# Kernel tuning notes

Hardware: AMD Instinct MI355X
Metric: run time of the kernel (lower is better)

## Reference

```python
import jax, jax.numpy as jnp
import numpy as np

B, N, K, D, H = 16384, 10, 5, 512, 2
HD = D // H  # 256
IMG = 512.0


def setup_inputs() -> dict:
    key = jax.random.key(0)
    ks = jax.random.split(key, 18)
    w = lambda k, shape: (jax.random.normal(k, shape) * 0.02).astype(jnp.float32)
    boxes = jax.random.uniform(ks[0], (B, N, 4), minval=0.0, maxval=IMG, dtype=jnp.float32)
    return {
        'boxes': boxes,
        'w_in': w(ks[1], (D, K * 4)), 'b_in': jnp.zeros((D,), jnp.float32),
        'wqkv': w(ks[2], (3 * D, D)), 'bqkv': jnp.zeros((3 * D,), jnp.float32),
        'wo': w(ks[3], (D, D)), 'bo': jnp.zeros((D,), jnp.float32),
        'ln1_w': jnp.ones((D,), jnp.float32), 'ln1_b': jnp.zeros((D,), jnp.float32),
        'w1': w(ks[4], (D, D)), 'b1': jnp.zeros((D,), jnp.float32),
        'w2': w(ks[5], (D, D)), 'b2': jnp.zeros((D,), jnp.float32),
        'ln2_w': jnp.ones((D,), jnp.float32), 'ln2_b': jnp.zeros((D,), jnp.float32),
        'lnf_w': jnp.ones((D,), jnp.float32), 'lnf_b': jnp.zeros((D,), jnp.float32),
    }


def _ln(x, w, b, eps=1e-5):
    mu = jnp.mean(x, -1, keepdims=True)
    var = jnp.mean((x - mu) ** 2, -1, keepdims=True)
    return (x - mu) * jax.lax.rsqrt(var + eps) * w + b


def _relationships(boxes):
    # boxes: [B, N, 4] -> rel: [B, N, K*4]
    cx = (boxes[..., 0] + boxes[..., 2]) * 0.5 / IMG
    cy = (boxes[..., 1] + boxes[..., 3]) * 0.5 / IMG
    bw = jnp.abs(boxes[..., 2] - boxes[..., 0]) / IMG
    bh = jnp.abs(boxes[..., 3] - boxes[..., 1]) / IMG
    feats = jnp.stack([cx, cy, bw, bh], -1)  # [B, N, 4]
    dx = cx[:, :, None] - cx[:, None, :]
    dy = cy[:, :, None] - cy[:, None, :]
    dists = dx * dx + dy * dy  # [B, N, N]
    dists = jnp.where(jnp.eye(N, dtype=bool), jnp.inf, dists)
    _, idx = jax.lax.top_k(-dists, K)  # K smallest, ascending -> [B, N, K]
    nbr = jnp.take_along_axis(jnp.broadcast_to(feats[:, None], (B, N, N, 4)), idx[:, :, :, None], axis=2)  # [B, N, K, 4]
    return (nbr - feats[:, :, None, :]).reshape(B, N, K * 4)


def reference(boxes, w_in, b_in, wqkv, bqkv, wo, bo, ln1_w, ln1_b, w1, b1, w2, b2, ln2_w, ln2_b, lnf_w, lnf_b):
    rel = _relationships(boxes)                      # [B, N, 20]
    x = rel @ w_in.T + b_in                          # [B, N, D]
    # --- self attention (post-norm TransformerEncoderLayer, eval mode: no dropout) ---
    qkv = x @ wqkv.T + bqkv
    q, k, v = jnp.split(qkv, 3, axis=-1)
    split_heads = lambda t: t.reshape(B, N, H, HD).transpose(0, 2, 1, 3)
    q, k, v = split_heads(q), split_heads(k), split_heads(v)
    scores = jnp.einsum('bhqd,bhkd->bhqk', q, k) / jnp.sqrt(jnp.float32(HD))
    att = jax.nn.softmax(scores, axis=-1)
    o = jnp.einsum('bhqk,bhkd->bhqd', att, v).transpose(0, 2, 1, 3).reshape(B, N, D)
    x = _ln(x + o @ wo.T + bo, ln1_w, ln1_b)
    # --- feed forward ---
    ff = jax.nn.gelu(x @ w1.T + b1, approximate=False) @ w2.T + b2
    x = _ln(x + ff, ln2_w, ln2_b)
    return _ln(x, lnf_w, lnf_b)
```

## Files before the change

### kernel.cpp

```cpp
#include <hip/hip_runtime.h>
#include <hip/hip_bf16.h>
#include <math.h>

#define B_   16384
#define NT   10
#define KNN  5
#define D_   512
#define MTOT (B_*NT)

typedef __bf16 bf;
typedef __bf16 bfrag8 __attribute__((ext_vector_type(8)));
typedef float  floatx4 __attribute__((ext_vector_type(4)));

__device__ __forceinline__ float tof(bf x) { return (float)x; }
__device__ __forceinline__ bf    tob(float x) { return (bf)x; }

#define GLD_LDS(g, l) __builtin_amdgcn_global_load_lds( \
    (const __attribute__((address_space(1))) void*)(g), \
    (__attribute__((address_space(3))) void*)(l), 16, 0, 0)

__global__ void prep_folds(const float* __restrict__ wqkv, const float* __restrict__ bqkv,
                           const float* __restrict__ wo,   const float* __restrict__ bo,
                           bf* __restrict__ At, bf* __restrict__ Ct,
                           float* __restrict__ wconst, float* __restrict__ uvec)
{
    int gid = blockIdx.x, tid = threadIdx.x;
    if (gid < 4096) {
        int idx = gid * 256 + tid;
        int mat = idx >> 18;
        int rem = idx & 262143;
        int row = rem >> 9, col = rem & 511;
        float acc = 0.f;
        if (mat < 2) {
            int h = mat;
            const float* wq = wqkv + (size_t)(h * 256) * 512;
            const float* wk = wqkv + (size_t)(512 + h * 256) * 512;
            for (int c = 0; c < 256; ++c)
                acc += wq[c * 512 + col] * wk[c * 512 + row];
            At[(size_t)h * 262144 + row * 512 + col] = tob(acc * 0.0625f);
        } else {
            int h = mat - 2;
            const float* wv = wqkv + (size_t)(1024 + h * 256) * 512;
            for (int e = 0; e < 256; ++e)
                acc += wv[e * 512 + col] * wo[row * 512 + h * 256 + e];
            Ct[(size_t)h * 262144 + row * 512 + col] = tob(acc);
        }
    } else {
        for (int d = tid; d < 512; d += 256) {
            float acc = bo[d];
            for (int e = 0; e < 512; ++e)
                acc += bqkv[1024 + e] * wo[d * 512 + e];
            wconst[d] = acc;
            for (int h = 0; h < 2; ++h) {
                float u = 0.f;
                for (int c = 0; c < 256; ++c)
                    u += wqkv[(size_t)(512 + h * 256 + c) * 512 + d] * bqkv[h * 256 + c];
                uvec[h * 512 + d] = u * 0.0625f;
            }
        }
    }
}

__global__ void cvt_w(const float* __restrict__ src, bf* __restrict__ dst)
{
    int i = blockIdx.x * 256 + threadIdx.x;
    float4 v = *(const float4*)(src + (size_t)i * 4);
    bf o[4] = { tob(v.x), tob(v.y), tob(v.z), tob(v.w) };
    *(unsigned long long*)(dst + (size_t)i * 4) = *(unsigned long long*)o;
}

__global__ void rel_kernel(const float* __restrict__ boxes, float* __restrict__ rel)
{
#pragma clang fp contract(off)
    int gid = blockIdx.x * blockDim.x + threadIdx.x;
    if (gid >= MTOT) return;
    int b = gid / NT, n = gid % NT;
    const float* bx = boxes + (size_t)b * NT * 4;
    float cx[NT], cy[NT], bw[NT], bh[NT];
#pragma unroll
    for (int j = 0; j < NT; ++j) {
        float x0 = bx[j * 4 + 0], y0 = bx[j * 4 + 1];
        float x1 = bx[j * 4 + 2], y1 = bx[j * 4 + 3];
        cx[j] = ((x0 + x1) * 0.5f) * (1.f / 512.f);
        cy[j] = ((y0 + y1) * 0.5f) * (1.f / 512.f);
        bw[j] = fabsf(x1 - x0) * (1.f / 512.f);
        bh[j] = fabsf(y1 - y0) * (1.f / 512.f);
    }
    float dist[NT];
#pragma unroll
    for (int j = 0; j < NT; ++j) {
        float dx = cx[n] - cx[j], dy = cy[n] - cy[j];
        float dxx = dx * dx, dyy = dy * dy;
        dist[j] = (j == n) ? __builtin_inff() : (dxx + dyy);
    }
    float ocx = cx[n], ocy = cy[n], obw = bw[n], obh = bh[n];
#pragma unroll
    for (int k = 0; k < KNN; ++k) {
        int best = 0; float bd = __builtin_inff();
#pragma unroll
        for (int j = 0; j < NT; ++j)
            if (dist[j] < bd) { bd = dist[j]; best = j; }
        float fx = 0, fy = 0, fw = 0, fh = 0;
#pragma unroll
        for (int j = 0; j < NT; ++j)
            if (j == best) { fx = cx[j]; fy = cy[j]; fw = bw[j]; fh = bh[j]; dist[j] = __builtin_inff(); }
        size_t o = (size_t)gid * 20 + k * 4;
        rel[o + 0] = fx - ocx;
        rel[o + 1] = fy - ocy;
        rel[o + 2] = fw - obw;
        rel[o + 3] = fh - obh;
    }
}

__global__ void gemm_in(const float* __restrict__ rel, const float* __restrict__ w_in,
                        const float* __restrict__ b_in, bf* __restrict__ x0)
{
    __shared__ __align__(16) float relS[128][20];
    int tid = threadIdx.x;
    size_t tok0 = (size_t)blockIdx.x * 128;
    for (int i = tid; i < 128 * 20; i += 256)
        relS[i / 20][i % 20] = rel[tok0 * 20 + i];
    float w0[20], w1r[20];
#pragma unroll
    for (int j = 0; j < 20; ++j) {
        w0[j]  = w_in[tid * 20 + j];
        w1r[j] = w_in[(tid + 256) * 20 + j];
    }
    float bias0 = b_in[tid], bias1 = b_in[tid + 256];
    __syncthreads();
    for (int tk = 0; tk < 128; ++tk) {
        const float4* rp = (const float4*)relS[tk];
        float a0 = bias0, a1 = bias1;
#pragma unroll
        for (int v4 = 0; v4 < 5; ++v4) {
            float4 rv = rp[v4];
            a0 += rv.x * w0[v4 * 4 + 0] + rv.y * w0[v4 * 4 + 1]
                + rv.z * w0[v4 * 4 + 2] + rv.w * w0[v4 * 4 + 3];
            a1 += rv.x * w1r[v4 * 4 + 0] + rv.y * w1r[v4 * 4 + 1]
                + rv.z * w1r[v4 * 4 + 2] + rv.w * w1r[v4 * 4 + 3];
        }
        x0[(tok0 + tk) * 512 + tid]       = tob(a0);
        x0[(tok0 + tk) * 512 + tid + 256] = tob(a1);
    }
}

template <int EPI>
__launch_bounds__(512, 4)
__global__ void gemm2(const bf* __restrict__ A, const bf* __restrict__ Bt,
                      bf* __restrict__ out, const float* __restrict__ biasf)
{
    __shared__ __align__(16) bf As[2][4096];
    __shared__ __align__(16) bf Bs[2][8192];
    int tid = threadIdx.x;
    int w = tid >> 6, l = tid & 63;
    int lq = l >> 4, lr = l & 15;
    size_t m0 = (size_t)blockIdx.y * 128;
    int n0 = blockIdx.x * 256;
    int wm = (w & 1) * 64, wn = (w >> 1) * 64;
    floatx4 acc[4][4] = {};

    const bf* Ag = A + (m0 + (size_t)(tid & 127)) * 512 + (tid >> 7) * 8;
    const bf* Bg = Bt + (size_t)(n0 + (tid & 255)) * 512 + (tid >> 8) * 8;

    auto stage = [&](int buf, int kt) {
        GLD_LDS(Ag + kt * 32,      &As[buf][w * 512]);
        GLD_LDS(Bg + kt * 32,      &Bs[buf][w * 512]);
        GLD_LDS(Bg + kt * 32 + 16, &Bs[buf][4096 + w * 512]);
    };

    stage(0, 0);
#pragma unroll 2
    for (int kt = 0; kt < 16; ++kt) {
        int cur = kt & 1;
        if (kt < 15) {
            stage(cur ^ 1, kt + 1);
            asm volatile("s_waitcnt vmcnt(3)" ::: "memory");
        } else {
            asm volatile("s_waitcnt vmcnt(0)" ::: "memory");
        }
        __builtin_amdgcn_sched_barrier(0);
        __builtin_amdgcn_s_barrier();
        __builtin_amdgcn_sched_barrier(0);

        const bf* as = &As[cur][(lq * 128 + wm + lr) * 8];
        const bf* bs = &Bs[cur][(lq * 256 + wn + lr) * 8];
        bfrag8 af[4], bfv[4];
#pragma unroll
        for (int i = 0; i < 4; ++i) af[i] = *(const bfrag8*)(as + i * 128);
#pragma unroll
        for (int j = 0; j < 4; ++j) bfv[j] = *(const bfrag8*)(bs + j * 128);
#pragma unroll
        for (int i = 0; i < 4; ++i)
#pragma unroll
            for (int j = 0; j < 4; ++j)
                acc[i][j] = __builtin_amdgcn_mfma_f32_16x16x32_bf16(af[i], bfv[j], acc[i][j], 0, 0, 0);

        if (kt < 15) {
            __builtin_amdgcn_sched_barrier(0);
            __builtin_amdgcn_s_barrier();
        }
    }

#pragma unroll
    for (int i = 0; i < 4; ++i)
#pragma unroll
        for (int j = 0; j < 4; ++j) {
            int col = n0 + wn + j * 16 + lr;
#pragma unroll
            for (int r = 0; r < 4; ++r) {
                size_t row = m0 + wm + i * 16 + lq * 4 + r;
                float v = acc[i][j][r];
                if (EPI == 1) { v += biasf[col]; v = 0.5f * v * (1.f + erff(v * 0.70710678118654752f)); }
                if (EPI == 2) v += biasf[col];
                if (EPI == 3) v += tof(out[row * 512 + col]);
                out[row * 512 + col] = tob(v);
            }
        }
}

__global__ void scoresz(bf* __restrict__ t, const bf* __restrict__ x0,
                        const float* __restrict__ uvec_h)
{
    __shared__ float as[4][256];
    int tid = threadIdx.x;
    int w = tid >> 6, l = tid & 63;
    int lq = l >> 4, lr = l & 15;
    size_t b = (size_t)blockIdx.x * 4 + w;
    bf* trow = t + (b * NT + lr) * 512;
    const bf* xrow = x0 + (b * NT + lr) * 512;
    floatx4 acc = {0.f, 0.f, 0.f, 0.f};
    float xu = 0.f;
#pragma unroll
    for (int kk = 0; kk < 16; ++kk) {
        bfrag8 a  = *(const bfrag8*)(trow + kk * 32 + lq * 8);
        bfrag8 bb = *(const bfrag8*)(xrow + kk * 32 + lq * 8);
        acc = __builtin_amdgcn_mfma_f32_16x16x32_bf16(a, bb, acc, 0, 0, 0);
#pragma unroll
        for (int jj = 0; jj < 8; ++jj)
            xu += (float)bb[jj] * uvec_h[kk * 32 + lq * 8 + jj];
    }
    xu += __shfl_xor(xu, 16);
    xu += __shfl_xor(xu, 32);
    bool jvalid = (lr < NT);
#pragma unroll
    for (int r = 0; r < 4; ++r) {
        float v = jvalid ? (acc[r] + xu) : -__builtin_inff();
        float m = v;
        m = fmaxf(m, __shfl_xor(m, 1)); m = fmaxf(m, __shfl_xor(m, 2));
        m = fmaxf(m, __shfl_xor(m, 4)); m = fmaxf(m, __shfl_xor(m, 8));
        float e = jvalid ? __expf(v - m) : 0.f;
        float s = e;
        s += __shfl_xor(s, 1); s += __shfl_xor(s, 2);
        s += __shfl_xor(s, 4); s += __shfl_xor(s, 8);
        float a = e / s;
        as[w][(lq * 4 + r) * 16 + lr] = a;
    }
    __syncthreads();
    bfrag8 xj[NT];
#pragma unroll
    for (int j = 0; j < NT; ++j)
        xj[j] = *(const bfrag8*)(x0 + (b * NT + j) * 512 + l * 8);
#pragma unroll
    for (int i = 0; i < NT; ++i) {
        float z[8] = {};
#pragma unroll
        for (int j = 0; j < NT; ++j) {
            float a = as[w][i * 16 + j];
#pragma unroll
            for (int q = 0; q < 8; ++q) z[q] += a * (float)xj[j][q];
        }
        bfrag8 zv;
#pragma unroll
        for (int q = 0; q < 8; ++q) zv[q] = tob(z[q]);
        *(bfrag8*)(t + (b * NT + i) * 512 + l * 8) = zv;
    }
}

__global__ void ln_kernel(const bf* __restrict__ xin, const bf* __restrict__ yin,
                          const float* __restrict__ w, const float* __restrict__ bias,
                          bf* __restrict__ xout)
{
    int tid = threadIdx.x;
    int wv = tid >> 6, l = tid & 63;
    size_t tok = (size_t)blockIdx.x * 4 + wv;
    bfrag8 xv = *(const bfrag8*)(xin + tok * 512 + l * 8);
    bfrag8 yv = *(const bfrag8*)(yin + tok * 512 + l * 8);
    float v[8]; float s = 0.f;
#pragma unroll
    for (int i = 0; i < 8; ++i) { v[i] = (float)xv[i] + (float)yv[i]; s += v[i]; }
#pragma unroll
    for (int m = 1; m < 64; m <<= 1) s += __shfl_xor(s, m);
    float mu = s * (1.f / 512.f);
    float vs = 0.f;
#pragma unroll
    for (int i = 0; i < 8; ++i) { float d = v[i] - mu; vs += d * d; }
#pragma unroll
    for (int m = 1; m < 64; m <<= 1) vs += __shfl_xor(vs, m);
    float r = rsqrtf(vs * (1.f / 512.f) + 1e-5f);
    bfrag8 ov;
#pragma unroll
    for (int i = 0; i < 8; ++i) {
        int d = l * 8 + i;
        ov[i] = tob((v[i] - mu) * r * w[d] + bias[d]);
    }
    *(bfrag8*)(xout + tok * 512 + l * 8) = ov;
}

__global__ void final_kernel(const bf* __restrict__ x1, const bf* __restrict__ ff2,
                             const float* __restrict__ w2, const float* __restrict__ b2,
                             const float* __restrict__ wf, const float* __restrict__ bfi,
                             float* __restrict__ out)
{
    int tid = threadIdx.x;
    int wv = tid >> 6, l = tid & 63;
    size_t tok = (size_t)blockIdx.x * 4 + wv;
    bfrag8 xv = *(const bfrag8*)(x1 + tok * 512 + l * 8);
    bfrag8 yv = *(const bfrag8*)(ff2 + tok * 512 + l * 8);
    float v[8]; float s = 0.f;
#pragma unroll
    for (int i = 0; i < 8; ++i) { v[i] = (float)xv[i] + (float)yv[i]; s += v[i]; }
#pragma unroll
    for (int m = 1; m < 64; m <<= 1) s += __shfl_xor(s, m);
    float mu = s * (1.f / 512.f);
    float vs = 0.f;
#pragma unroll
    for (int i = 0; i < 8; ++i) { float d = v[i] - mu; vs += d * d; }
#pragma unroll
    for (int m = 1; m < 64; m <<= 1) vs += __shfl_xor(vs, m);
    float r = rsqrtf(vs * (1.f / 512.f) + 1e-5f);
    float u[8]; float s2 = 0.f;
#pragma unroll
    for (int i = 0; i < 8; ++i) {
        int d = l * 8 + i;
        u[i] = (v[i] - mu) * r * w2[d] + b2[d];
        s2 += u[i];
    }
#pragma unroll
    for (int m = 1; m < 64; m <<= 1) s2 += __shfl_xor(s2, m);
    float mu2 = s2 * (1.f / 512.f);
    float vs2 = 0.f;
#pragma unroll
    for (int i = 0; i < 8; ++i) { float d = u[i] - mu2; vs2 += d * d; }
#pragma unroll
    for (int m = 1; m < 64; m <<= 1) vs2 += __shfl_xor(vs2, m);
    float r2 = rsqrtf(vs2 * (1.f / 512.f) + 1e-5f);
    float4 o0, o1;
    float* op = (float*)&o0;
#pragma unroll
    for (int i = 0; i < 4; ++i) op[i] = (u[i] - mu2) * r2 * wf[l * 8 + i] + bfi[l * 8 + i];
    op = (float*)&o1;
#pragma unroll
    for (int i = 0; i < 4; ++i) op[i] = (u[4 + i] - mu2) * r2 * wf[l * 8 + 4 + i] + bfi[l * 8 + 4 + i];
    *(float4*)(out + tok * 512 + l * 8) = o0;
    *(float4*)(out + tok * 512 + l * 8 + 4) = o1;
}

extern "C" void kernel_launch(void* const* d_in, const int* in_sizes, int n_in,
                              void* d_out, int out_size, void* d_ws, size_t ws_size,
                              hipStream_t stream)
{
    const float* boxes = (const float*)d_in[0];
    const float* w_in  = (const float*)d_in[1];
    const float* b_in  = (const float*)d_in[2];
    const float* wqkv  = (const float*)d_in[3];
    const float* bqkv  = (const float*)d_in[4];
    const float* wo    = (const float*)d_in[5];
    const float* bo    = (const float*)d_in[6];
    const float* ln1w  = (const float*)d_in[7];
    const float* ln1b  = (const float*)d_in[8];
    const float* w1    = (const float*)d_in[9];
    const float* b1    = (const float*)d_in[10];
    const float* w2    = (const float*)d_in[11];
    const float* b2    = (const float*)d_in[12];
    const float* ln2w  = (const float*)d_in[13];
    const float* ln2b  = (const float*)d_in[14];
    const float* lnfw  = (const float*)d_in[15];
    const float* lnfb  = (const float*)d_in[16];
    float* out = (float*)d_out;

    char* ws = (char*)d_ws;
    bf*    At     = (bf*)(ws + 0);
    bf*    Ct     = (bf*)(ws + 1048576);
    bf*    W1b    = (bf*)(ws + 2097152);
    bf*    W2b    = (bf*)(ws + 2621440);
    float* wconst = (float*)(ws + 3145728);
    float* uvec   = (float*)(ws + 3147776);
    bf*    x0     = (bf*)(ws + 16259072);
    bf*    t      = (bf*)(ws + 184047616);
    bf*    y      = (bf*)(ws + 351836160);
    float* rel    = (float*)(ws + 184047616);

    dim3 gblk(256);
    dim3 ggemm(2, MTOT / 128);

    prep_folds<<<4097, gblk, 0, stream>>>(wqkv, bqkv, wo, bo, At, Ct, wconst, uvec);
    cvt_w<<<256, gblk, 0, stream>>>(w1, W1b);
    cvt_w<<<256, gblk, 0, stream>>>(w2, W2b);
    rel_kernel<<<(MTOT + 255) / 256, gblk, 0, stream>>>(boxes, rel);
    gemm_in<<<MTOT / 128, gblk, 0, stream>>>(rel, w_in, b_in, x0);

    gemm2<0><<<ggemm, 512, 0, stream>>>(x0, At, t, nullptr);
    scoresz<<<B_ / 4, gblk, 0, stream>>>(t, x0, uvec);
    gemm2<2><<<ggemm, 512, 0, stream>>>(t, Ct, y, wconst);
    gemm2<0><<<ggemm, 512, 0, stream>>>(x0, At + 262144, t, nullptr);
    scoresz<<<B_ / 4, gblk, 0, stream>>>(t, x0, uvec + 512);
    gemm2<3><<<ggemm, 512, 0, stream>>>(t, Ct + 262144, y, nullptr);
    ln_kernel<<<MTOT / 4, gblk, 0, stream>>>(x0, y, ln1w, ln1b, x0);
    gemm2<1><<<ggemm, 512, 0, stream>>>(x0, W1b, t, b1);
    gemm2<2><<<ggemm, 512, 0, stream>>>(t, W2b, y, b2);
    final_kernel<<<MTOT / 4, gblk, 0, stream>>>(x0, y, ln2w, ln2b, lnfw, lnfb, out);
}
```

Before: 2.172 ms.

## Triple-buffer GEMM LDS staging and drop the trailing per-iteration barrier

Changes the bf16 MFMA GEMM from double to triple LDS buffering, issuing global-to-LDS loads two k-tiles ahead right after the single barrier and removing the second barrier in each iteration. LDS fragment reads become explicit ds_read_b128 with an lgkmcnt wait, and wave priority is raised around the MFMA block. This is meant to hide load latency and cut barrier stalls. The larger LDS footprint (72KB per block) may reduce how many blocks fit on each CU.

```diff
diff --git a/kernel.cpp b/kernel.cpp
--- a/kernel.cpp
+++ b/kernel.cpp
@@ -18,6 +18,13 @@
 #define GLD_LDS(g, l) __builtin_amdgcn_global_load_lds( \
     (const __attribute__((address_space(1))) void*)(g), \
     (__attribute__((address_space(3))) void*)(l), 16, 0, 0)
+
+__device__ __forceinline__ bfrag8 lds_read16(const bf* p) {
+    bfrag8 r;
+    unsigned a = (unsigned)(unsigned long long)(const __attribute__((address_space(3))) bf*)p;
+    asm volatile("ds_read_b128 %0, %1" : "=v"(r) : "v"(a));
+    return r;
+}
 
 __global__ void prep_folds(const float* __restrict__ wqkv, const float* __restrict__ bqkv,
                            const float* __restrict__ wo,   const float* __restrict__ bo,
@@ -146,11 +153,11 @@
 
 template <int EPI>
 __launch_bounds__(512, 4)
-__global__ void gemm2(const bf* __restrict__ A, const bf* __restrict__ Bt,
+__global__ void gemm3(const bf* __restrict__ A, const bf* __restrict__ Bt,
                       bf* __restrict__ out, const float* __restrict__ biasf)
 {
-    __shared__ __align__(16) bf As[2][4096];
-    __shared__ __align__(16) bf Bs[2][8192];
+    __shared__ __align__(16) bf As[3][4096];
+    __shared__ __align__(16) bf Bs[3][8192];
     int tid = threadIdx.x;
     int w = tid >> 6, l = tid & 63;
     int lq = l >> 4, lr = l & 15;
@@ -169,11 +176,10 @@
     };
 
     stage(0, 0);
-#pragma unroll 2
+    stage(1, 1);
+    int cur = 0;
     for (int kt = 0; kt < 16; ++kt) {
-        int cur = kt & 1;
         if (kt < 15) {
-            stage(cur ^ 1, kt + 1);
             asm volatile("s_waitcnt vmcnt(3)" ::: "memory");
         } else {
             asm volatile("s_waitcnt vmcnt(0)" ::: "memory");
@@ -182,23 +188,29 @@
         __builtin_amdgcn_s_barrier();
         __builtin_amdgcn_sched_barrier(0);
 
+        if (kt < 14) {
+            int nb = cur + 2; if (nb >= 3) nb -= 3;
+            stage(nb, kt + 2);
+        }
+
         const bf* as = &As[cur][(lq * 128 + wm + lr) * 8];
         const bf* bs = &Bs[cur][(lq * 256 + wn + lr) * 8];
         bfrag8 af[4], bfv[4];
 #pragma unroll
-        for (int i = 0; i < 4; ++i) af[i] = *(const bfrag8*)(as + i * 128);
-#pragma unroll
-        for (int j = 0; j < 4; ++j) bfv[j] = *(const bfrag8*)(bs + j * 128);
+        for (int i = 0; i < 4; ++i) af[i] = lds_read16(as + i * 128);
+#pragma unroll
+        for (int j = 0; j < 4; ++j) bfv[j] = lds_read16(bs + j * 128);
+        asm volatile("s_waitcnt lgkmcnt(0)" ::: "memory");
+        __builtin_amdgcn_sched_barrier(0);
+        __builtin_amdgcn_s_setprio(1);
 #pragma unroll
         for (int i = 0; i < 4; ++i)
 #pragma unroll
             for (int j = 0; j < 4; ++j)
                 acc[i][j] = __builtin_amdgcn_mfma_f32_16x16x32_bf16(af[i], bfv[j], acc[i][j], 0, 0, 0);
-
-        if (kt < 15) {
-            __builtin_amdgcn_sched_barrier(0);
-            __builtin_amdgcn_s_barrier();
-        }
+        __builtin_amdgcn_s_setprio(0);
+
+        cur = (cur == 2) ? 0 : cur + 1;
     }
 
 #pragma unroll
@@ -399,14 +411,14 @@
     rel_kernel<<<(MTOT + 255) / 256, gblk, 0, stream>>>(boxes, rel);
     gemm_in<<<MTOT / 128, gblk, 0, stream>>>(rel, w_in, b_in, x0);
 
-    gemm2<0><<<ggemm, 512, 0, stream>>>(x0, At, t, nullptr);
+    gemm3<0><<<ggemm, 512, 0, stream>>>(x0, At, t, nullptr);
     scoresz<<<B_ / 4, gblk, 0, stream>>>(t, x0, uvec);
-    gemm2<2><<<ggemm, 512, 0, stream>>>(t, Ct, y, wconst);
-    gemm2<0><<<ggemm, 512, 0, stream>>>(x0, At + 262144, t, nullptr);
+    gemm3<2><<<ggemm, 512, 0, stream>>>(t, Ct, y, wconst);
+    gemm3<0><<<ggemm, 512, 0, stream>>>(x0, At + 262144, t, nullptr);
     scoresz<<<B_ / 4, gblk, 0, stream>>>(t, x0, uvec + 512);
-    gemm2<3><<<ggemm, 512, 0, stream>>>(t, Ct + 262144, y, nullptr);
+    gemm3<3><<<ggemm, 512, 0, stream>>>(t, Ct + 262144, y, nullptr);
     ln_kernel<<<MTOT / 4, gblk, 0, stream>>>(x0, y, ln1w, ln1b, x0);
-    gemm2<1><<<ggemm, 512, 0, stream>>>(x0, W1b, t, b1);
-    gemm2<2><<<ggemm, 512, 0, stream>>>(t, W2b, y, b2);
+    gemm3<1><<<ggemm, 512, 0, stream>>>(x0, W1b, t, b1);
+    gemm3<2><<<ggemm, 512, 0, stream>>>(t, W2b, y, b2);
     final_kernel<<<MTOT / 4, gblk, 0, stream>>>(x0, y, ln2w, ln2b, lnfw, lnfb, out);
 }
```

Measured after the change: 2.197 ms. About the same (+1.2%).
